# Optimization experiments

Measured on AMD Instinct MI355X. Metric: run time of the kernel, lower is better.

The kernel has to match this reference:

```python
import jax, jax.numpy as jnp
import numpy as np

RATE = 2
KSIZE = 3          # patch size for similarity
KERNEL = 2 * RATE  # patch size for alpha scatter (4)
BN_EPS = 1e-5


def _extract_patches(x, k, s):
    """Mirror of GuidedCxtAtten.extract_patches: reflect-pad then unfold.
    x: [B,C,H,W] -> [B,Ho,Wo,C,k,k] with Ho=H//s, Wo=W//s."""
    left = (k - s + 1) // 2
    right = (k - s) // 2
    xp = jnp.pad(x, ((0, 0), (0, 0), (left, right), (left, right)), mode='reflect')
    Hp, Wp = xp.shape[2], xp.shape[3]
    Ho = (Hp - k) // s + 1
    Wo = (Wp - k) // s + 1
    ii = (jnp.arange(Ho) * s)[:, None] + jnp.arange(k)[None, :]   # [Ho,k]
    jj = (jnp.arange(Wo) * s)[:, None] + jnp.arange(k)[None, :]   # [Wo,k]
    p = xp[:, :, ii[:, :, None, None], jj[None, None, :, :]]      # [B,C,Ho,k,Wo,k]
    return p.transpose(0, 2, 4, 1, 3, 5)                          # [B,Ho,Wo,C,k,k]


def setup_inputs() -> dict:
    key = jax.random.key(0)
    ks = jax.random.split(key, 5)
    B, Cg, Ca, H, W = 4, 256, 128, 128, 128
    f = jax.random.normal(ks[0], (B, Cg, H, W), dtype=jnp.float32)
    alpha = jax.random.normal(ks[1], (B, Ca, H, W), dtype=jnp.float32)
    unknown = (jax.random.uniform(ks[2], (B, 1, H, W)) > 0.5).astype(jnp.float32)
    # guidance_conv: 1x1, Cg -> Cg//2, xavier-ish
    gc_w = jax.random.normal(ks[3], (Cg // 2, Cg), dtype=jnp.float32) * np.sqrt(2.0 / (Cg + Cg // 2))
    gc_b = jnp.zeros((Cg // 2,), dtype=jnp.float32)
    # W[0]: 1x1 conv Ca->Ca no bias; W[1]: BN with gamma=0.001, beta=0 per init
    w_w = jax.random.normal(ks[4], (Ca, Ca), dtype=jnp.float32) * np.sqrt(1.0 / Ca)
    bn_gamma = jnp.full((Ca,), 0.001, dtype=jnp.float32)
    bn_beta = jnp.zeros((Ca,), dtype=jnp.float32)
    return {"f": f, "alpha": alpha, "unknown": unknown, "gc_w": gc_w, "gc_b": gc_b,
            "w_w": w_w, "bn_gamma": bn_gamma, "bn_beta": bn_beta}


def _forward(f, alpha, unknown, gc_w, gc_b, w_w, bn_gamma, bn_beta):
    # guidance 1x1 conv
    fg = jnp.einsum('oi,bihw->bohw', gc_w, f) + gc_b[None, :, None, None]
    B, _, H, W = fg.shape
    Ca = alpha.shape[1]
    Hs, Ws = H // RATE, W // RATE
    L = Hs * Ws

    # alpha patches [B,L,Ca,4,4] (kernel=2*rate, stride=rate)
    alpha_w = _extract_patches(alpha, KERNEL, RATE).reshape(B, L, Ca, KERNEL, KERNEL)

    # nearest downsample by rate (torch nearest with scale 1/2 == strided pick)
    f_ds = fg[:, :, ::RATE, ::RATE]                # [B,Cg/2,Hs,Ws]
    unk_ds = unknown[:, :, ::RATE, ::RATE]         # [B,1,Hs,Ws]

    # similarity filter patches [B,L,C,3,3]
    w = _extract_patches(f_ds, KSIZE, 1).reshape(B, L, -1, KSIZE, KSIZE)

    # known/unknown softmax scales [B,2]
    u_mean = unk_ds.mean(axis=(2, 3))              # [B,1]
    k_mean = 1.0 - u_mean
    su = jnp.clip(jnp.sqrt(u_mean / k_mean), 0.1, 10.0)
    sk = jnp.clip(jnp.sqrt(k_mean / u_mean), 0.1, 10.0)
    softmax_scale = jnp.concatenate([su, sk], axis=1)

    # patch-mean of unknown mask -> binary patch mask [B,L]
    m = _extract_patches(unk_ds, KSIZE, 1).reshape(B, L, -1).mean(axis=2)
    mm = (m > 0.0).astype(fg.dtype)

    # l2-normalize filters per patch, then correlate against all positions.
    # Conv of reflect-padded f_ds with stride-1 3x3 patch filters == inner
    # product of normalized patches with the raw patches (same extraction).
    norm = jnp.sqrt(jnp.sum(w * w, axis=(2, 3, 4), keepdims=True))
    w_normed = w / jnp.maximum(norm, 1e-4)
    scores = jnp.einsum('bqcij,bpcij->bqp', w_normed, w)   # [B,L(q=patch),L(p=pos)]

    # known/unknown scaling per source patch q
    gate = jnp.where(mm > 0.0, su, sk)                      # [B,L]
    scores = scores * gate[:, :, None]

    # self-match suppression only for unknown patches (diagonal q == p)
    diag = jnp.arange(L)
    scores = scores.at[:, diag, diag].add(-10000.0 * mm)

    attn = jax.nn.softmax(scores, axis=1)                   # softmax over patches q

    # offsets (argmax patch per position, relative to center)
    idx = jnp.argmax(attn, axis=1)                          # [B,L]
    offsets = jnp.stack([idx // Ws, idx % Ws], axis=1).reshape(B, 2, Hs, Ws)
    offsets = offsets - jnp.array([Hs // 2, Ws // 2]).reshape(1, 2, 1, 1)

    # scatter alpha patches with attention weights: per-sample conv_transpose2d
    attn_map = attn.reshape(B, L, Hs, Ws)

    def ct(yi, wc):  # yi [L,Hs,Ws], wc [L,Ca,4,4]
        rhs = jnp.flip(wc, (2, 3)).transpose(1, 0, 2, 3)    # [Ca,L,4,4]
        pad = KERNEL - 1 - 1                                # torch padding=1
        out = jax.lax.conv_general_dilated(
            yi[None], rhs, window_strides=(1, 1),
            padding=[(pad, pad), (pad, pad)], lhs_dilation=(RATE, RATE),
            dimension_numbers=('NCHW', 'OIHW', 'NCHW'))
        return out[0]

    y = jax.vmap(ct)(attn_map, alpha_w) / 4.0               # [B,Ca,H,W]

    # W: 1x1 conv (no bias) + BatchNorm2d (training-mode batch stats)
    yw = jnp.einsum('oi,bihw->bohw', w_w, y)
    mean = yw.mean(axis=(0, 2, 3))
    var = yw.var(axis=(0, 2, 3))
    yn = (yw - mean[None, :, None, None]) * jax.lax.rsqrt(var + BN_EPS)[None, :, None, None]
    yn = yn * bn_gamma[None, :, None, None] + bn_beta[None, :, None, None]

    return yn + alpha, offsets, softmax_scale


def reference(f, alpha, unknown, gc_w, gc_b, w_w, bn_gamma, bn_beta):
    return _forward(f, alpha, unknown, gc_w, gc_b, w_w, bn_gamma, bn_beta)
```

## Files before the change

### kernel.cpp

```cpp
#include <hip/hip_runtime.h>
#include <math.h>

#define B 4
#define CG 256
#define CM 128
#define CA 128
#define H 128
#define W_ 128
#define HS 64
#define WS 64
#define L 4096
#define D1 1152
#define D2 2048
#define NPIX 65536
#define NT1 36
#define NT2 128

#define STP_F 8388608UL
#define RA_F  4194304UL
#define SLOT_F (STP_F + RA_F + RA_F)

typedef unsigned short u16;
typedef __attribute__((ext_vector_type(8))) short short8v;
typedef __attribute__((ext_vector_type(4))) unsigned short u16x4;
typedef __attribute__((ext_vector_type(4))) float f32x4;

__device__ __forceinline__ float bf2f(u16 x) {
    union { unsigned int u; float f; } v; v.u = ((unsigned int)x) << 16; return v.f;
}
__device__ __forceinline__ u16 f2bf(float x) {
    union { float f; unsigned int u; } v; v.f = x;
    unsigned int r = (v.u + 0x7FFFu + ((v.u >> 16) & 1u)) >> 16;
    return (u16)r;
}
__device__ __forceinline__ void gll16(const void* g, void* l) {
    __builtin_amdgcn_global_load_lds((const __attribute__((address_space(1))) void*)g,
                                     (__attribute__((address_space(3))) void*)l, 16, 0, 0);
}
__device__ __forceinline__ int refl(int i, int n) {
    return i < 0 ? -i : (i >= n ? 2 * n - 2 - i : i);
}
__device__ __forceinline__ int swz(int row, int fq) {
    return row * 32 + ((fq ^ ((row >> 1) & 3)) * 8);
}
__device__ __forceinline__ short8v rdfrag32(const char* lds, int r, int fq) {
    return *(const short8v*)(lds + r * 64 + ((fq * 16) ^ (((r >> 1) & 3) << 4)));
}

__global__ __launch_bounds__(256) void k_conv_ds(const float* __restrict__ f,
                                                 const float* __restrict__ gw,
                                                 const float* __restrict__ gb,
                                                 float* __restrict__ fds,
                                                 float* __restrict__ ssq) {
    __shared__ float sf[CG * 64];
    __shared__ float part[4][64];
    int t = threadIdx.x;
    int hs = blockIdx.x, b = blockIdx.y;
    const float* fb = f + (size_t)b * CG * H * W_ + (2 * hs) * W_;
    for (int idx = t; idx < CG * 64; idx += 256) {
        int ci = idx >> 6, ws = idx & 63;
        sf[idx] = fb[(size_t)ci * H * W_ + 2 * ws];
    }
    __syncthreads();
    int ws = t & 63;
    int wave = __builtin_amdgcn_readfirstlane(t >> 6);
    const float* gwp = gw + (size_t)(wave * 32) * CG;
    float acc[32];
#pragma unroll
    for (int r = 0; r < 32; ++r) acc[r] = gb[wave * 32 + r];
    for (int ci = 0; ci < CG; ++ci) {
        float fv = sf[ci * 64 + ws];
#pragma unroll
        for (int r = 0; r < 32; ++r) acc[r] += gwp[r * CG + ci] * fv;
    }
    float sq = 0.f;
#pragma unroll
    for (int r = 0; r < 32; ++r) {
        int co = wave * 32 + r;
        fds[(((size_t)b * CM + co) * HS + hs) * WS + ws] = acc[r];
        sq += acc[r] * acc[r];
    }
    part[wave][ws] = sq;
    __syncthreads();
    if (t < 64)
        ssq[((size_t)b * HS + hs) * WS + t] =
            part[0][t] + part[1][t] + part[2][t] + part[3][t];
}

__global__ __launch_bounds__(256) void k_scale(const float* __restrict__ unk,
                                               float* __restrict__ suk,
                                               float* __restrict__ out2) {
    int b = blockIdx.x, t = threadIdx.x;
    __shared__ float red[256];
    float s = 0.f;
    for (int i = t; i < L; i += 256) {
        int hs = i >> 6, ws = i & 63;
        s += unk[(size_t)b * H * W_ + (2 * hs) * W_ + 2 * ws];
    }
    red[t] = s;
    __syncthreads();
    for (int o = 128; o > 0; o >>= 1) {
        if (t < o) red[t] += red[t + o];
        __syncthreads();
    }
    if (t == 0) {
        float u = red[0] / (float)L;
        float k = 1.0f - u;
        float su = sqrtf(u / k); su = fminf(fmaxf(su, 0.1f), 10.0f);
        float sk = sqrtf(k / u); sk = fminf(fmaxf(sk, 0.1f), 10.0f);
        suk[b * 2] = su; suk[b * 2 + 1] = sk;
        out2[b * 2] = su; out2[b * 2 + 1] = sk;
    }
}

__global__ __launch_bounds__(64) void k_gate(const float* __restrict__ unk,
                                             const float* __restrict__ ssq,
                                             const float* __restrict__ suk,
                                             float* __restrict__ g,
                                             float* __restrict__ dg) {
    int ws = threadIdx.x, hs = blockIdx.x, b = blockIdx.y;
    float sm = 0.f, sq = 0.f;
    for (int di = -1; di <= 1; ++di) {
        int rh = refl(hs + di, HS);
        for (int dj = -1; dj <= 1; ++dj) {
            int rw = refl(ws + dj, WS);
            sm += unk[(size_t)b * H * W_ + (2 * rh) * W_ + 2 * rw];
            sq += ssq[((size_t)b * HS + rh) * WS + rw];
        }
    }
    float mm   = (sm > 0.0f) ? 1.0f : 0.0f;
    float norm = sqrtf(sq);
    float gate = (mm > 0.0f) ? suk[2 * b] : suk[2 * b + 1];
    int q = hs * WS + ws;
    g[(size_t)b * L + q]  = gate / fmaxf(norm, 1e-4f);
    dg[(size_t)b * L + q] = -10000.0f * mm;
}

__global__ __launch_bounds__(256) void k_buildW(const float* __restrict__ fds,
                                                float* __restrict__ base, int b0) {
    int bz = blockIdx.z;
    int b  = b0 + bz;
    u16* Whi = (u16*)(base + (size_t)bz * SLOT_F + STP_F);
    int ws = threadIdx.x;
    int c  = blockIdx.y * 4 + threadIdx.y;
    int hs = blockIdx.x;
    int q = hs * WS + ws;
    size_t bo = (size_t)q * D1 + c * 9;
    const float* src = fds + ((size_t)b * CM + c) * HS * WS;
#pragma unroll
    for (int i = 0; i < 3; ++i) {
        int rh = refl(hs + i - 1, HS);
#pragma unroll
        for (int j = 0; j < 3; ++j) {
            int rw = refl(ws + j - 1, WS);
            Whi[bo + i * 3 + j] = f2bf(src[rh * WS + rw]);
        }
    }
}

__global__ __launch_bounds__(256, 3) void k_gemm1(float* __restrict__ base,
                                                  const float* __restrict__ g0,
                                                  const float* __restrict__ dg0,
                                                  int b0) {
    __shared__ u16 sA[3][128 * 32], sB[3][128 * 32];
    int bz = blockIdx.z;
    float* S = base + (size_t)bz * SLOT_F;
    u16* STP = (u16*)S;
    const u16* Whi = (const u16*)(S + STP_F);
    const float* g  = g0  + (size_t)(b0 + bz) * L;
    const float* dg = dg0 + (size_t)(b0 + bz) * L;

    int tid = threadIdx.x;
    int wv = tid >> 6, lane = tid & 63;
    int t0 = blockIdx.x, I = 0;
    while (t0 >= 32 - I) { t0 -= 32 - I; ++I; }
    int J = I + t0;
    int pTile = I * 128, qTile = J * 128;
    int wp = (wv >> 1) * 64, wq = (wv & 1) * 64;
    int r0 = wv * 32;
    int lrow = lane >> 2;
    int csw = ((lane & 3) ^ ((lrow >> 1) & 3)) * 8;
    int fr = lane & 15, fq = lane >> 4;

    const u16* gArow = Whi + (size_t)(pTile + r0 + lrow) * D1 + csw;
    const u16* gBrow = Whi + (size_t)(qTile + r0 + lrow) * D1 + csw;

#define G1STG(kt, bf) do { \
    gll16(gArow + (kt) * 32, &sA[bf][r0 * 32]); \
    gll16(gArow + (kt) * 32 + (size_t)16 * D1, &sA[bf][(r0 + 16) * 32]); \
    gll16(gBrow + (kt) * 32, &sB[bf][r0 * 32]); \
    gll16(gBrow + (kt) * 32 + (size_t)16 * D1, &sB[bf][(r0 + 16) * 32]); } while (0)

#define G1PHASE(t, ca, cb, na, nb_) do { \
    int nxb = ((t) + 1) % 3; \
    _Pragma("unroll") for (int i = 0; i < 4; ++i) \
        nb_[i] = *(const short8v*)&sB[nxb][swz(wq + i * 16 + fr, fq)]; \
    __builtin_amdgcn_s_setprio(1); \
    _Pragma("unroll") for (int mi = 0; mi < 2; ++mi) \
        _Pragma("unroll") for (int ni = 0; ni < 4; ++ni) \
            acc[mi][ni] = __builtin_amdgcn_mfma_f32_16x16x32_bf16(ca[mi], cb[ni], acc[mi][ni], 0, 0, 0); \
    __builtin_amdgcn_s_setprio(0); \
    _Pragma("unroll") for (int i = 0; i < 4; ++i) \
        na[i] = *(const short8v*)&sA[nxb][swz(wp + i * 16 + fr, fq)]; \
    G1STG(((t) + 3 < NT1) ? (t) + 3 : 0, (t) % 3); \
    asm volatile("s_waitcnt vmcnt(4)" ::: "memory"); \
    __builtin_amdgcn_s_setprio(1); \
    _Pragma("unroll") for (int mi = 2; mi < 4; ++mi) \
        _Pragma("unroll") for (int ni = 0; ni < 4; ++ni) \
            acc[mi][ni] = __builtin_amdgcn_mfma_f32_16x16x32_bf16(ca[mi], cb[ni], acc[mi][ni], 0, 0, 0); \
    __builtin_amdgcn_s_setprio(0); \
    asm volatile("s_waitcnt lgkmcnt(0)" ::: "memory"); \
    __builtin_amdgcn_s_barrier(); \
    __builtin_amdgcn_sched_barrier(0); } while (0)

    f32x4 acc[4][4];
#pragma unroll
    for (int mi = 0; mi < 4; ++mi)
#pragma unroll
        for (int ni = 0; ni < 4; ++ni)
#pragma unroll
            for (int r = 0; r < 4; ++r) acc[mi][ni][r] = 0.f;

    G1STG(0, 0);
    G1STG(1, 1);
    G1STG(2, 2);
    asm volatile("s_waitcnt vmcnt(4)" ::: "memory");
    __builtin_amdgcn_s_barrier();
    __builtin_amdgcn_sched_barrier(0);

    short8v fa0[4], fb0[4], fa1[4], fb1[4];
#pragma unroll
    for (int i = 0; i < 4; ++i) {
        fa0[i] = *(const short8v*)&sA[0][swz(wp + i * 16 + fr, fq)];
        fb0[i] = *(const short8v*)&sB[0][swz(wq + i * 16 + fr, fq)];
    }
    asm volatile("s_waitcnt lgkmcnt(0)" ::: "memory");
    __builtin_amdgcn_s_barrier();
    __builtin_amdgcn_sched_barrier(0);

    for (int t = 0; t < NT1; t += 2) {
        G1PHASE(t,     fa0, fb0, fa1, fb1);
        G1PHASE(t + 1, fa1, fb1, fa0, fb0);
    }
#undef G1PHASE
#undef G1STG

#pragma unroll
    for (int ni = 0; ni < 4; ++ni) {
        int qq = qTile + wq + ni * 16 + fr;
        float gq = g[qq];
        float dq = dg[qq];
#pragma unroll
        for (int mi = 0; mi < 4; ++mi) {
            int pB = pTile + wp + mi * 16 + fq * 4;
#pragma unroll
            for (int r = 0; r < 4; ++r) {
                int p = pB + r;
                float v = acc[mi][ni][r] * gq;
                if (p == qq) v += dq;
                STP[(size_t)p * L + qq] = f2bf(v);
            }
        }
    }
    if (I != J) {
#pragma unroll
        for (int mi = 0; mi < 4; ++mi) {
            int p0 = pTile + wp + mi * 16 + fq * 4;
            float gp0 = g[p0], gp1 = g[p0 + 1], gp2 = g[p0 + 2], gp3 = g[p0 + 3];
#pragma unroll
            for (int ni = 0; ni < 4; ++ni) {
                int qq = qTile + wq + ni * 16 + fr;
                u16x4 mv;
                mv[0] = f2bf(acc[mi][ni][0] * gp0);
                mv[1] = f2bf(acc[mi][ni][1] * gp1);
                mv[2] = f2bf(acc[mi][ni][2] * gp2);
                mv[3] = f2bf(acc[mi][ni][3] * gp3);
                *(u16x4*)(STP + (size_t)qq * L + p0) = mv;
            }
        }
    }
}

__global__ __launch_bounds__(256) void k_softmax(float* __restrict__ base,
                                                 const float* __restrict__ fds,
                                                 const float* __restrict__ g0,
                                                 const float* __restrict__ dg0,
                                                 float* __restrict__ out1, int b0) {
    __shared__ float buf[L];
    __shared__ float wmax[4], wsum[4], cred[4];
    __shared__ int candList[128];
    __shared__ int candCount;
    int bz = blockIdx.y;
    int b  = b0 + bz;
    float* S = base + (size_t)bz * SLOT_F;
    u16* STP = (u16*)S;
    const float* fdsb = fds + (size_t)b * CM * HS * WS;
    const float* g  = g0  + (size_t)b * L;
    const float* dg = dg0 + (size_t)b * L;

    int p = blockIdx.x, t = threadIdx.x;
    int lane = t & 63, wv = t >> 6;
    u16* rowp = STP + (size_t)p * L;

    if (t == 0) candCount = 0;
    float mx = -3.4e38f;
    for (int i = t; i < L / 8; i += 256) {
        short8v v8 = ((const short8v*)rowp)[i];
#pragma unroll
        for (int j = 0; j < 8; ++j) {
            float v = bf2f((u16)v8[j]);
            buf[i * 8 + j] = v;
            mx = fmaxf(mx, v);
        }
    }
#pragma unroll
    for (int o = 32; o > 0; o >>= 1) mx = fmaxf(mx, __shfl_xor(mx, o));
    if (lane == 0) wmax[wv] = mx;
    __syncthreads();
    float M = fmaxf(fmaxf(wmax[0], wmax[1]), fmaxf(wmax[2], wmax[3]));
    float cth = M - (fabsf(M) * 0.0625f + 1e-5f);

    float s = 0.f;
    for (int i = t; i < L; i += 256) {
        float v = buf[i];
        if (v >= cth) {
            int ix = atomicAdd(&candCount, 1);
            if (ix < 128) candList[ix] = i;
        }
        float e = __expf(v - M);
        buf[i] = e;
        s += e;
    }
#pragma unroll
    for (int o = 32; o > 0; o >>= 1) s += __shfl_xor(s, o);
    if (lane == 0) wsum[wv] = s;
    __syncthreads();
    float inv = 1.0f / (wsum[0] + wsum[1] + wsum[2] + wsum[3]);

    for (int i = t; i < L / 8; i += 256) {
        short8v o8;
#pragma unroll
        for (int j = 0; j < 8; ++j) o8[j] = (short)f2bf(buf[i * 8 + j] * inv);
        ((short8v*)rowp)[i] = o8;
    }

    int nc = candCount; if (nc > 128) nc = 128;
    int bestI;
    if (nc == 1) {
        bestI = candList[0];
    } else {
        float bestE = -3.4e38f; bestI = L;
        int hp = p >> 6, wpp = p & 63;
        for (int k = 0; k < nc; ++k) {
            int cand = candList[k];
            int hc = cand >> 6, wcc = cand & 63;
            float part = 0.f;
#pragma unroll
            for (int e = 0; e < 5; ++e) {
                int kk = t + e * 256;
                if (kk < D1) {
                    int c  = kk / 9, ij = kk - c * 9;
                    int di = ij / 3, dj = ij - di * 3;
                    float pv = fdsb[(size_t)c * (HS * WS)
                                    + refl(hp + di - 1, HS) * WS + refl(wpp + dj - 1, WS)];
                    float cv = fdsb[(size_t)c * (HS * WS)
                                    + refl(hc + di - 1, HS) * WS + refl(wcc + dj - 1, WS)];
                    part += pv * cv;
                }
            }
#pragma unroll
            for (int o = 32; o > 0; o >>= 1) part += __shfl_xor(part, o);
            if (lane == 0) cred[wv] = part;
            __syncthreads();
            float e1 = (cred[0] + cred[1] + cred[2] + cred[3]) * g[cand]
                     + (p == cand ? dg[cand] : 0.f);
            if (e1 > bestE || (e1 == bestE && cand < bestI)) { bestE = e1; bestI = cand; }
            __syncthreads();
        }
    }
    if (t == 0) {
        out1[(size_t)(b * 2 + 0) * L + p] = (float)(bestI / WS - 32);
        out1[(size_t)(b * 2 + 1) * L + p] = (float)(bestI % WS - 32);
    }
}

__global__ __launch_bounds__(256) void k_buildA(const float* __restrict__ alpha,
                                                float* __restrict__ base, int b0) {
    int bz = blockIdx.z;
    int b  = b0 + bz;
    u16* At = (u16*)(base + (size_t)bz * SLOT_F + STP_F);
    int q = blockIdx.x * 256 + threadIdx.x;
    int n = blockIdx.y;
    int hs = q >> 6, ws = q & 63;
    int c = n >> 4, ki = (n >> 2) & 3, kj = n & 3;
    int rh = refl(2 * hs + ki - 1, H);
    int rw = refl(2 * ws + kj - 1, W_);
    At[(size_t)n * L + q] = f2bf(alpha[((size_t)b * CA + c) * H * W_ + rh * W_ + rw]);
}

__global__ __launch_bounds__(512, 2) void k_gemm2(float* __restrict__ base) {
    __shared__ u16 smem[65536];
    char* sm = (char*)smem;
    int bz = blockIdx.z;
    float* S = base + (size_t)bz * SLOT_F;
    const u16* P  = (const u16*)S;
    const u16* At = (const u16*)(S + STP_F);
    u16* Z        = (u16*)(S + STP_F + RA_F);

    int tid = threadIdx.x;
    int wid = tid >> 6, lane = tid & 63;
    int wm = wid >> 2, wn = wid & 3;
    int pTile = blockIdx.x * 256, nTile = blockIdx.y * 256;
    int fr = lane & 15, fq = lane >> 4;

    int off0 = wid * 1024 + lane * 16;
    int row0 = off0 >> 6, cb0 = off0 & 63;
    int off1 = off0 + 8192;
    int row1 = off1 >> 6, cb1 = off1 & 63;
    const u16* pA0 = P  + (size_t)(pTile + row0) * L + ((cb0 ^ (((row0 >> 1) & 3) << 4)) >> 1);
    const u16* pA1 = P  + (size_t)(pTile + row1) * L + ((cb1 ^ (((row1 >> 1) & 3) << 4)) >> 1);
    const u16* pB0 = At + (size_t)(nTile + row0) * L + ((cb0 ^ (((row0 >> 1) & 3) << 4)) >> 1);
    const u16* pB1 = At + (size_t)(nTile + row1) * L + ((cb1 ^ (((row1 >> 1) & 3) << 4)) >> 1);

#define STG2(kt, bi) do { \
    char* d = sm + (bi) * 32768 + wid * 1024; \
    gll16(pA0 + (size_t)(kt) * 32, d); \
    gll16(pA1 + (size_t)(kt) * 32, d + 8192); \
    gll16(pB0 + (size_t)(kt) * 32, d + 16384); \
    gll16(pB1 + (size_t)(kt) * 32, d + 24576); } while (0)

#define PRELOAD2(fa, fb, bi) do { \
    const char* Ab_ = sm + (bi) * 32768; \
    const char* Bb_ = Ab_ + 16384; \
    _Pragma("unroll") for (int n = 0; n < 4; ++n) fb[n] = rdfrag32(Bb_, wn * 64 + n * 16 + fr, fq); \
    _Pragma("unroll") for (int m = 0; m < 8; ++m) fa[m] = rdfrag32(Ab_, wm * 128 + m * 16 + fr, fq); } while (0)

#define PHASE2(t, ca, cb, na, nb_) do { \
    const char* Abn = sm + (((t) + 1) & 3) * 32768; \
    const char* Bbn = Abn + 16384; \
    _Pragma("unroll") for (int n = 0; n < 4; ++n) nb_[n] = rdfrag32(Bbn, wn * 64 + n * 16 + fr, fq); \
    __builtin_amdgcn_s_setprio(1); \
    _Pragma("unroll") for (int m = 0; m < 4; ++m) \
        _Pragma("unroll") for (int n = 0; n < 4; ++n) \
            acc[m][n] = __builtin_amdgcn_mfma_f32_16x16x32_bf16(ca[m], cb[n], acc[m][n], 0, 0, 0); \
    __builtin_amdgcn_s_setprio(0); \
    _Pragma("unroll") for (int m = 0; m < 8; ++m) na[m] = rdfrag32(Abn, wm * 128 + m * 16 + fr, fq); \
    STG2(((t) + 3 < NT2) ? (t) + 3 : 0, ((t) + 3) & 3); \
    asm volatile("s_waitcnt vmcnt(4)" ::: "memory"); \
    __builtin_amdgcn_s_setprio(1); \
    _Pragma("unroll") for (int m = 4; m < 8; ++m) \
        _Pragma("unroll") for (int n = 0; n < 4; ++n) \
            acc[m][n] = __builtin_amdgcn_mfma_f32_16x16x32_bf16(ca[m], cb[n], acc[m][n], 0, 0, 0); \
    __builtin_amdgcn_s_setprio(0); \
    asm volatile("s_waitcnt lgkmcnt(0)" ::: "memory"); \
    __builtin_amdgcn_s_barrier(); \
    __builtin_amdgcn_sched_barrier(0); } while (0)

    f32x4 acc[8][4];
#pragma unroll
    for (int m = 0; m < 8; ++m)
#pragma unroll
        for (int n = 0; n < 4; ++n)
#pragma unroll
            for (int r = 0; r < 4; ++r) acc[m][n][r] = 0.f;

    STG2(0, 0);
    STG2(1, 1);
    STG2(2, 2);
    asm volatile("s_waitcnt vmcnt(4)" ::: "memory");
    __builtin_amdgcn_s_barrier();
    __builtin_amdgcn_sched_barrier(0);

    short8v fa0[8], fb0[4], fa1[8], fb1[4];
    PRELOAD2(fa0, fb0, 0);
    asm volatile("s_waitcnt lgkmcnt(0)" ::: "memory");
    __builtin_amdgcn_sched_barrier(0);

    for (int t = 0; t < NT2; t += 2) {
        PHASE2(t,     fa0, fb0, fa1, fb1);
        PHASE2(t + 1, fa1, fb1, fa0, fb0);
    }
#undef PHASE2
#undef PRELOAD2
#undef STG2

#pragma unroll
    for (int m = 0; m < 8; ++m)
#pragma unroll
        for (int n = 0; n < 4; ++n) {
            int nn = nTile + wn * 64 + n * 16 + fr;
#pragma unroll
            for (int r = 0; r < 4; ++r) {
                int pp = pTile + wm * 128 + m * 16 + fq * 4 + r;
                Z[(size_t)pp * D2 + nn] = f2bf(acc[m][n][r]);
            }
        }
}

__global__ __launch_bounds__(256) void k_gather(float* __restrict__ base,
                                                u16* __restrict__ yt, int b0) {
    int bz = blockIdx.z;
    int b  = b0 + bz;
    const u16* Z = (const u16*)(base + (size_t)bz * SLOT_F + STP_F + RA_F);
    int c  = threadIdx.x & 127;
    int pl = threadIdx.x >> 7;
    int w  = blockIdx.x * 2 + pl;
    int h  = blockIdx.y;
    float s = 0.f;
#pragma unroll
    for (int ki = 0; ki < 4; ++ki) {
        int num = h + 1 - ki;
        if (num < 0 || (num & 1)) continue;
        int hs = num >> 1;
        if (hs >= HS) continue;
#pragma unroll
        for (int kj = 0; kj < 4; ++kj) {
            int numw = w + 1 - kj;
            if (numw < 0 || (numw & 1)) continue;
            int wsd = numw >> 1;
            if (wsd >= WS) continue;
            s += bf2f(Z[(size_t)(hs * WS + wsd) * D2 + c * 16 + ki * 4 + kj]);
        }
    }
    int pix = h * W_ + w;
    int cs = c ^ ((pix & 7) << 3);
    yt[((size_t)b * 16384 + pix) * 128 + cs] = f2bf(0.25f * s);
}

__global__ __launch_bounds__(256) void k_cvtww(const float* __restrict__ ww,
                                               u16* __restrict__ wwbf) {
    int i = blockIdx.x * 256 + threadIdx.x;
    int o = i >> 7, c = i & 127;
    wwbf[o * 128 + (c ^ ((o & 7) << 3))] = f2bf(ww[i]);
}

__global__ __launch_bounds__(256) void k_ywgemm(const u16* __restrict__ wwbf,
                                                const u16* __restrict__ yt,
                                                float* __restrict__ yw) {
    __shared__ u16 sA[128 * 128], sB[128 * 128];
    int tid = threadIdx.x;
    int wv = tid >> 6, lane = tid & 63;
    int nTile = blockIdx.x * 128;
    int wp = (wv >> 1) * 64, wn = (wv & 1) * 64;
    int fr = lane & 15, fq = lane >> 4;

    const u16* gB = yt + (size_t)nTile * 128;
#pragma unroll
    for (int i = 0; i < 8; ++i) {
        int o = (i * 4 + wv) * 512;
        gll16(wwbf + o + lane * 8, &sA[o]);
        gll16(gB + o + lane * 8, &sB[o]);
    }
    __syncthreads();

    f32x4 acc[4][4];
#pragma unroll
    for (int mi = 0; mi < 4; ++mi)
#pragma unroll
        for (int ni = 0; ni < 4; ++ni)
#pragma unroll
            for (int r = 0; r < 4; ++r) acc[mi][ni][r] = 0.f;

#pragma unroll
    for (int ks = 0; ks < 4; ++ks) {
        int k0 = ks * 32 + fq * 8;
        short8v a[4], bb[4];
#pragma unroll
        for (int i = 0; i < 4; ++i) {
            int ra = wp + i * 16 + fr;
            a[i] = *(const short8v*)&sA[ra * 128 + (k0 ^ ((ra & 7) << 3))];
            int rb = wn + i * 16 + fr;
            bb[i] = *(const short8v*)&sB[rb * 128 + (k0 ^ ((rb & 7) << 3))];
        }
#pragma unroll
        for (int mi = 0; mi < 4; ++mi)
#pragma unroll
            for (int ni = 0; ni < 4; ++ni)
                acc[mi][ni] = __builtin_amdgcn_mfma_f32_16x16x32_bf16(a[mi], bb[ni], acc[mi][ni], 0, 0, 0);
    }

#pragma unroll
    for (int mi = 0; mi < 4; ++mi)
#pragma unroll
        for (int ni = 0; ni < 4; ++ni) {
            int gp = nTile + wn + ni * 16 + fr;
#pragma unroll
            for (int r = 0; r < 4; ++r) {
                int o = wp + mi * 16 + fq * 4 + r;
                yw[(size_t)o * NPIX + gp] = acc[mi][ni][r];
            }
        }
}

__global__ __launch_bounds__(256) void k_stats(const float* __restrict__ yw,
                                               float* __restrict__ meanvar) {
    int o = blockIdx.x, t = threadIdx.x;
    __shared__ float rs[256], rq[256];
    float s = 0.f, q = 0.f;
    const float* p = yw + (size_t)o * NPIX;
    for (int i = t; i < NPIX; i += 256) {
        float v = p[i];
        s += v;
        q += v * v;
    }
    rs[t] = s; rq[t] = q;
    __syncthreads();
    for (int off = 128; off > 0; off >>= 1) {
        if (t < off) { rs[t] += rs[t + off]; rq[t] += rq[t + off]; }
        __syncthreads();
    }
    if (t == 0) {
        float n = (float)NPIX;
        float mean = rs[0] / n;
        float var  = rq[0] / n - mean * mean;
        meanvar[o] = mean;
        meanvar[CA + o] = var;
    }
}

__global__ __launch_bounds__(256) void k_final(const float* __restrict__ yw,
                                               const float* __restrict__ meanvar,
                                               const float* __restrict__ gamma,
                                               const float* __restrict__ beta,
                                               const float* __restrict__ alpha,
                                               float* __restrict__ out0) {
    size_t i = ((size_t)blockIdx.x * 256 + threadIdx.x) * 4;
    int c = (int)((i >> 14) & 127);
    int b = (int)(i >> 21);
    int pix = (int)(i & 16383);
    float4 v = *(const float4*)(yw + (size_t)c * NPIX + b * 16384 + pix);
    float4 a = *(const float4*)(alpha + i);
    float mean = meanvar[c];
    float var  = meanvar[CA + c];
    float sc   = rsqrtf(var + 1e-5f) * gamma[c];
    float bt   = beta[c];
    float4 r;
    r.x = (v.x - mean) * sc + bt + a.x;
    r.y = (v.y - mean) * sc + bt + a.y;
    r.z = (v.z - mean) * sc + bt + a.z;
    r.w = (v.w - mean) * sc + bt + a.w;
    *(float4*)(out0 + i) = r;
}

extern "C" void kernel_launch(void* const* d_in, const int* in_sizes, int n_in,
                              void* d_out, int out_size, void* d_ws, size_t ws_size,
                              hipStream_t stream) {
    (void)in_sizes; (void)n_in; (void)out_size;
    const float* f     = (const float*)d_in[0];
    const float* alpha = (const float*)d_in[1];
    const float* unk   = (const float*)d_in[2];
    const float* gw    = (const float*)d_in[3];
    const float* gb    = (const float*)d_in[4];
    const float* ww    = (const float*)d_in[5];
    const float* gamma = (const float*)d_in[6];
    const float* beta  = (const float*)d_in[7];

    float* out0 = (float*)d_out;
    float* out1 = out0 + (size_t)B * CA * H * W_;
    float* out2 = out1 + (size_t)B * 2 * HS * WS;

    float* wsf = (float*)d_ws;
    size_t off = 0;
    float* fds     = wsf + off; off += (size_t)B * CM * HS * WS;
    float* ssq     = wsf + off; off += (size_t)B * HS * WS;
    float* gbuf    = wsf + off; off += (size_t)B * L;
    float* dgbuf   = wsf + off; off += (size_t)B * L;
    float* suk     = wsf + off; off += 64;
    float* ytF     = wsf + off; off += (size_t)NPIX * 128 / 2;
    float* wwbfF   = wsf + off; off += 8192;
    float* meanvar = wsf + off; off += 256;
    float* base    = wsf + off;

    const size_t PRE_F = off;
    int nb = (ws_size >= (PRE_F + 4 * SLOT_F) * sizeof(float)) ? 4 : 2;

    float* yw   = base;
    u16*   yt   = (u16*)ytF;
    u16*   wwbf = (u16*)wwbfF;

    k_cvtww<<<64, 256, 0, stream>>>(ww, wwbf);
    k_conv_ds<<<dim3(64, 4), 256, 0, stream>>>(f, gw, gb, fds, ssq);
    k_scale<<<4, 256, 0, stream>>>(unk, suk, out2);
    k_gate<<<dim3(64, 4), 64, 0, stream>>>(unk, ssq, suk, gbuf, dgbuf);

    for (int b0 = 0; b0 < B; b0 += nb) {
        k_buildW<<<dim3(64, 32, nb), dim3(64, 4), 0, stream>>>(fds, base, b0);
        k_gemm1<<<dim3(528, 1, nb), 256, 0, stream>>>(base, gbuf, dgbuf, b0);
        k_softmax<<<dim3(4096, nb), 256, 0, stream>>>(base, fds, gbuf, dgbuf, out1, b0);
        k_buildA<<<dim3(16, 2048, nb), 256, 0, stream>>>(alpha, base, b0);
        k_gemm2<<<dim3(16, 8, nb), 512, 0, stream>>>(base);
        k_gather<<<dim3(64, 128, nb), 256, 0, stream>>>(base, yt, b0);
    }

    k_ywgemm<<<512, 256, 0, stream>>>(wwbf, yt, yw);
    k_stats<<<128, 256, 0, stream>>>(yw, meanvar);
    k_final<<<8192, 256, 0, stream>>>(yw, meanvar, gamma, beta, alpha, out0);
}
```

Before: 829.9 us.

## Defer softmax normalization to gather and drop LDS row buffer; vectorize buildA

The softmax kernel no longer stages a 4096-float row in shared memory. It re-reads the bf16 row from global memory, writes unnormalized exponentials and stores the per-row sum. The gather kernel divides by that row sum, which removes a full pass over the row and frees 16KB of LDS for occupancy. buildA is reworked to write four values per thread with channel-major n indexing, and gather's Z indexing is changed to match. A barrier is also added after the gemm2 preload. The risk is extra reads and divides in gather, plus slightly different bf16 rounding because unnormalized values are stored.

```diff
diff --git a/kernel.cpp b/kernel.cpp
--- a/kernel.cpp
+++ b/kernel.cpp
@@ -285,8 +285,8 @@
                                                  const float* __restrict__ fds,
                                                  const float* __restrict__ g0,
                                                  const float* __restrict__ dg0,
+                                                 float* __restrict__ rowsum,
                                                  float* __restrict__ out1, int b0) {
-    __shared__ float buf[L];
     __shared__ float wmax[4], wsum[4], cred[4];
     __shared__ int candList[128];
     __shared__ int candCount;
@@ -307,11 +307,7 @@
     for (int i = t; i < L / 8; i += 256) {
         short8v v8 = ((const short8v*)rowp)[i];
 #pragma unroll
-        for (int j = 0; j < 8; ++j) {
-            float v = bf2f((u16)v8[j]);
-            buf[i * 8 + j] = v;
-            mx = fmaxf(mx, v);
-        }
+        for (int j = 0; j < 8; ++j) mx = fmaxf(mx, bf2f((u16)v8[j]));
     }
 #pragma unroll
     for (int o = 32; o > 0; o >>= 1) mx = fmaxf(mx, __shfl_xor(mx, o));
@@ -321,28 +317,27 @@
     float cth = M - (fabsf(M) * 0.0625f + 1e-5f);
 
     float s = 0.f;
-    for (int i = t; i < L; i += 256) {
-        float v = buf[i];
-        if (v >= cth) {
-            int ix = atomicAdd(&candCount, 1);
-            if (ix < 128) candList[ix] = i;
-        }
-        float e = __expf(v - M);
-        buf[i] = e;
-        s += e;
+    for (int i = t; i < L / 8; i += 256) {
+        short8v v8 = ((const short8v*)rowp)[i];
+        short8v o8;
+#pragma unroll
+        for (int j = 0; j < 8; ++j) {
+            float v = bf2f((u16)v8[j]);
+            if (v >= cth) {
+                int ix = atomicAdd(&candCount, 1);
+                if (ix < 128) candList[ix] = i * 8 + j;
+            }
+            float e = __expf(v - M);
+            o8[j] = (short)f2bf(e);
+            s += e;
+        }
+        ((short8v*)rowp)[i] = o8;
     }
 #pragma unroll
     for (int o = 32; o > 0; o >>= 1) s += __shfl_xor(s, o);
     if (lane == 0) wsum[wv] = s;
     __syncthreads();
-    float inv = 1.0f / (wsum[0] + wsum[1] + wsum[2] + wsum[3]);
-
-    for (int i = t; i < L / 8; i += 256) {
-        short8v o8;
-#pragma unroll
-        for (int j = 0; j < 8; ++j) o8[j] = (short)f2bf(buf[i * 8 + j] * inv);
-        ((short8v*)rowp)[i] = o8;
-    }
+    if (t == 0) rowsum[(size_t)b * L + p] = wsum[0] + wsum[1] + wsum[2] + wsum[3];
 
     int nc = candCount; if (nc > 128) nc = 128;
     int bestI;
@@ -389,13 +384,17 @@
     int bz = blockIdx.z;
     int b  = b0 + bz;
     u16* At = (u16*)(base + (size_t)bz * SLOT_F + STP_F);
-    int q = blockIdx.x * 256 + threadIdx.x;
-    int n = blockIdx.y;
-    int hs = q >> 6, ws = q & 63;
-    int c = n >> 4, ki = (n >> 2) & 3, kj = n & 3;
+    int q0 = (blockIdx.x * 256 + threadIdx.x) * 4;
+    int n  = blockIdx.y;
+    int c = n & 127, kikj = n >> 7, ki = kikj >> 2, kj = kikj & 3;
+    int hs = q0 >> 6, ws = q0 & 63;
     int rh = refl(2 * hs + ki - 1, H);
-    int rw = refl(2 * ws + kj - 1, W_);
-    At[(size_t)n * L + q] = f2bf(alpha[((size_t)b * CA + c) * H * W_ + rh * W_ + rw]);
+    const float* arow = alpha + ((size_t)b * CA + c) * H * W_ + rh * W_;
+    u16x4 ov;
+#pragma unroll
+    for (int j = 0; j < 4; ++j)
+        ov[j] = f2bf(arow[refl(2 * (ws + j) + kj - 1, W_)]);
+    *(u16x4*)(At + (size_t)n * L + q0) = ov;
 }
 
 __global__ __launch_bounds__(512, 2) void k_gemm2(float* __restrict__ base) {
@@ -474,6 +473,7 @@
     short8v fa0[8], fb0[4], fa1[8], fb1[4];
     PRELOAD2(fa0, fb0, 0);
     asm volatile("s_waitcnt lgkmcnt(0)" ::: "memory");
+    __builtin_amdgcn_s_barrier();
     __builtin_amdgcn_sched_barrier(0);
 
     for (int t = 0; t < NT2; t += 2) {
@@ -498,10 +498,12 @@
 }
 
 __global__ __launch_bounds__(256) void k_gather(float* __restrict__ base,
+                                                const float* __restrict__ rowsum,
                                                 u16* __restrict__ yt, int b0) {
     int bz = blockIdx.z;
     int b  = b0 + bz;
     const u16* Z = (const u16*)(base + (size_t)bz * SLOT_F + STP_F + RA_F);
+    const float* rs = rowsum + (size_t)b * L;
     int c  = threadIdx.x & 127;
     int pl = threadIdx.x >> 7;
     int w  = blockIdx.x * 2 + pl;
@@ -519,7 +521,8 @@
             if (numw < 0 || (numw & 1)) continue;
             int wsd = numw >> 1;
             if (wsd >= WS) continue;
-            s += bf2f(Z[(size_t)(hs * WS + wsd) * D2 + c * 16 + ki * 4 + kj]);
+            int src = hs * WS + wsd;
+            s += bf2f(Z[(size_t)src * D2 + (ki * 4 + kj) * 128 + c]) / rs[src];
         }
     }
     int pix = h * W_ + w;
@@ -669,6 +672,7 @@
     float* ytF     = wsf + off; off += (size_t)NPIX * 128 / 2;
     float* wwbfF   = wsf + off; off += 8192;
     float* meanvar = wsf + off; off += 256;
+    float* rowsum  = wsf + off; off += (size_t)B * L;
     float* base    = wsf + off;
 
     const size_t PRE_F = off;
@@ -686,10 +690,10 @@
     for (int b0 = 0; b0 < B; b0 += nb) {
         k_buildW<<<dim3(64, 32, nb), dim3(64, 4), 0, stream>>>(fds, base, b0);
         k_gemm1<<<dim3(528, 1, nb), 256, 0, stream>>>(base, gbuf, dgbuf, b0);
-        k_softmax<<<dim3(4096, nb), 256, 0, stream>>>(base, fds, gbuf, dgbuf, out1, b0);
-        k_buildA<<<dim3(16, 2048, nb), 256, 0, stream>>>(alpha, base, b0);
+        k_softmax<<<dim3(4096, nb), 256, 0, stream>>>(base, fds, gbuf, dgbuf, rowsum, out1, b0);
+        k_buildA<<<dim3(4, 2048, nb), 256, 0, stream>>>(alpha, base, b0);
         k_gemm2<<<dim3(16, 8, nb), 512, 0, stream>>>(base);
-        k_gather<<<dim3(64, 128, nb), 256, 0, stream>>>(base, yt, b0);
+        k_gather<<<dim3(64, 128, nb), 256, 0, stream>>>(base, rowsum, yt, b0);
     }
 
     k_ywgemm<<<512, 256, 0, stream>>>(wwbf, yt, yw);
```

Result: faster. 803.7 us (-3.2%).
